# Optimization experiments

Hardware: AMD Instinct MI355X
Metric: run time of the kernel (lower is better)

Reference implementation:

```python
import jax, jax.numpy as jnp
import numpy as np

N, E, F, H = 50000, 800000, 128, 128

def silu(v):
    return v * jax.nn.sigmoid(v)

def setup_inputs() -> dict:
    key = jax.random.key(0)
    ks = jax.random.split(key, 16)
    def lin(k, fan_in, fan_out):
        s = 1.0 / np.sqrt(fan_in)
        kw, kb = jax.random.split(k)
        W = jax.random.uniform(kw, (fan_in, fan_out), jnp.float32, -s, s)
        b = jax.random.uniform(kb, (fan_out,), jnp.float32, -s, s)
        return W, b
    x = jax.random.normal(ks[0], (N, F), jnp.float32)
    pos = jax.random.normal(ks[1], (N, 3), jnp.float32)
    edge_index = jax.random.randint(ks[2], (2, E), 0, N, jnp.int64)
    We1, be1 = lin(ks[3], 2 * F + 1, H)
    We2, be2 = lin(ks[4], H, H)
    Wn1, bn1 = lin(ks[5], F + H, H)
    Wn2, bn2 = lin(ks[6], H, F)
    Wc, bc = lin(ks[7], H, 1)
    return {"x": x, "pos": pos, "We1": We1, "be1": be1, "We2": We2, "be2": be2,
            "Wn1": Wn1, "bn1": bn1, "Wn2": Wn2, "bn2": bn2, "Wc": Wc, "bc": bc,
            "edge_index": edge_index}

def reference(x, pos, We1, be1, We2, be2, Wn1, bn1, Wn2, bn2, Wc, bc, edge_index):
    row, col = edge_index[0], edge_index[1]
    rij = pos[row] - pos[col]                      # [E,3]
    dij = jnp.sum(rij ** 2, axis=-1, keepdims=True)  # [E,1]
    edge_input = jnp.concatenate([x[row], x[col], dij], axis=-1)  # [E,2F+1]
    m_ij = silu(silu(edge_input @ We1 + be1) @ We2 + be2)          # [E,H]
    agg = jax.ops.segment_sum(m_ij, row, num_segments=N)          # [N,H]
    x_new = silu(jnp.concatenate([x, agg], axis=-1) @ Wn1 + bn1) @ Wn2 + bn2  # [N,F]
    w_ij = silu(m_ij @ Wc + bc)                    # [E,1]
    trans = rij * w_ij                             # [E,3]
    delta = jax.ops.segment_sum(trans, row, num_segments=N)       # [N,3]
    pos_new = pos + 0.01 * delta
    return (x_new, pos_new)
```

## Files before the change

### kernel.cpp

```cpp
#include <hip/hip_runtime.h>
#include <hip/hip_bf16.h>
#include <stdint.h>
#include <string.h>

#define NN 50000
#define NE 800000
#define SCAN_B 200
#define SCAN_CH 250

typedef short bf8_t __attribute__((ext_vector_type(8)));
typedef float f32x4 __attribute__((ext_vector_type(4)));

__device__ __forceinline__ float silu_f(float v) {
    return v * __builtin_amdgcn_rcpf(1.0f + __expf(-v));
}

__device__ __forceinline__ unsigned int pack2bf(float a, float b) {
    __hip_bfloat162 h = __float22bfloat162_rn(make_float2(a, b));
    unsigned int u; memcpy(&u, &h, 4);
    return u;
}

__device__ __forceinline__ float bf_lo(unsigned int u) { return __uint_as_float(u << 16); }
__device__ __forceinline__ float bf_hi(unsigned int u) { return __uint_as_float(u & 0xffff0000u); }

union U4B { uint4 u; bf8_t b; };
__device__ __forceinline__ bf8_t as_bf8(uint4 u) { U4B x; x.u = u; return x.b; }

__global__ __launch_bounds__(64) void prep_w(const float* __restrict__ We1,
                                             const float* __restrict__ We2,
                                             const float* __restrict__ Wn1,
                                             const float* __restrict__ Wn2,
                                             unsigned short* __restrict__ wf1,
                                             unsigned short* __restrict__ wf2,
                                             unsigned short* __restrict__ wfn1,
                                             unsigned short* __restrict__ wfn2) {
    int b = blockIdx.x, lane = threadIdx.x;
    int q = lane >> 4, c = lane & 15;
    const float* W; unsigned short* dst; int f;
    if (b < 64)       { W = We1; f = b;       dst = wf1  + (size_t)f * 512; }
    else if (b < 96)  { W = We2; f = b - 64;  dst = wf2  + (size_t)f * 512; }
    else if (b < 160) { W = Wn1; f = b - 96;  dst = wfn1 + (size_t)f * 512; }
    else              { W = Wn2; f = b - 160; dst = wfn2 + (size_t)f * 512; }
    int s = f >> 3, mf = f & 7;
    int k0 = s * 32 + q * 8, col = mf * 16 + c;
    float v[8];
    #pragma unroll
    for (int i = 0; i < 8; ++i) v[i] = W[(size_t)(k0 + i) * 128 + col];
    uint4 o;
    o.x = pack2bf(v[0], v[1]); o.y = pack2bf(v[2], v[3]);
    o.z = pack2bf(v[4], v[5]); o.w = pack2bf(v[6], v[7]);
    *(uint4*)(dst + lane * 8) = o;
}

__device__ __forceinline__ void node_gemm_pass(
    const float* __restrict__ x, const unsigned* nb, const int* nloc, int n0,
    const char* __restrict__ wbase, const float* __restrict__ bias,
    unsigned short* __restrict__ dst, int P, int lane, int q, int oc_q)
{
    f32x4 acc[2][4];
    #pragma unroll
    for (int M = 0; M < 2; ++M) {
        float4 bi = bias ? *(const float4*)(bias + oc_q + M * 16) : make_float4(0.f, 0.f, 0.f, 0.f);
        #pragma unroll
        for (int t = 0; t < 4; ++t) { acc[M][t][0] = bi.x; acc[M][t][1] = bi.y; acc[M][t][2] = bi.z; acc[M][t][3] = bi.w; }
    }
    #pragma unroll
    for (int s = 0; s < 4; ++s) {
        bf8_t bfr[4];
        #pragma unroll
        for (int t = 0; t < 4; ++t) {
            const float* src = x + ((size_t)nb[t]) * 128 + s * 32 + q * 8;
            float4 v0 = *(const float4*)src;
            float4 v1 = *(const float4*)(src + 4);
            uint4 o;
            o.x = pack2bf(v0.x, v0.y); o.y = pack2bf(v0.z, v0.w);
            o.z = pack2bf(v1.x, v1.y); o.w = pack2bf(v1.z, v1.w);
            bfr[t] = as_bf8(o);
        }
        #pragma unroll
        for (int M = 0; M < 2; ++M) {
            unsigned woff = ((unsigned)(s * 8 + P * 2 + M) << 10) + ((unsigned)lane << 4);
            bf8_t af = as_bf8(*(const uint4*)(wbase + woff));
            #pragma unroll
            for (int t = 0; t < 4; ++t)
                acc[M][t] = __builtin_amdgcn_mfma_f32_16x16x32_bf16(af, bfr[t], acc[M][t], 0, 0, 0);
        }
    }
    #pragma unroll
    for (int M = 0; M < 2; ++M) {
        #pragma unroll
        for (int t = 0; t < 4; ++t) {
            int node = n0 + nloc[t];
            if (node < NN) {
                uint2 pz;
                pz.x = pack2bf(acc[M][t][0], acc[M][t][1]);
                pz.y = pack2bf(acc[M][t][2], acc[M][t][3]);
                *(uint2*)(dst + ((size_t)node << 7) + oc_q + M * 16) = pz;
            }
        }
    }
}

__global__ __launch_bounds__(256, 2) void prep_node(
    const float* __restrict__ x, const int* __restrict__ ei,
    const unsigned short* __restrict__ wf1, const unsigned short* __restrict__ wfn1,
    const float* __restrict__ be1, const float* __restrict__ bn1,
    unsigned short* __restrict__ zbf, unsigned short* __restrict__ ybf,
    unsigned short* __restrict__ znbf, int* __restrict__ cnt)
{
    const int tid = threadIdx.x;
    const int n0 = blockIdx.x * 64;

    {
        int e0 = (blockIdx.x * 256 + tid) * 4;
        if (e0 < NE) {
            int4 r4 = *(const int4*)(ei + e0);
            atomicAdd(&cnt[r4.x], 1); atomicAdd(&cnt[r4.y], 1);
            atomicAdd(&cnt[r4.z], 1); atomicAdd(&cnt[r4.w], 1);
        }
    }

    const int P = tid >> 6, lane = tid & 63;
    const int q = lane >> 4, e16 = lane & 15;
    const int oc_q = P * 32 + q * 4;

    int nloc[4]; unsigned nb[4];
    #pragma unroll
    for (int t = 0; t < 4; ++t) {
        int nl = t * 16 + e16; nloc[t] = nl;
        int node = n0 + nl; if (node >= NN) node = NN - 1;
        nb[t] = (unsigned)node;
    }

    node_gemm_pass(x, nb, nloc, n0, (const char*)wf1,           be1, zbf,  P, lane, q, oc_q);
    node_gemm_pass(x, nb, nloc, n0, (const char*)wf1 + (32u << 10), nullptr, ybf, P, lane, q, oc_q);
    node_gemm_pass(x, nb, nloc, n0, (const char*)wfn1,          bn1, znbf, P, lane, q, oc_q);
}

__global__ __launch_bounds__(256) void scan_bsum(const int* __restrict__ cnt,
                                                 int* __restrict__ bsum) {
    __shared__ int red[4];
    int b = blockIdx.x, tid = threadIdx.x;
    int n = b * SCAN_CH + tid;
    int v = (tid < SCAN_CH) ? cnt[n] : 0;
    #pragma unroll
    for (int o = 32; o; o >>= 1) v += __shfl_down(v, o);
    if ((tid & 63) == 0) red[tid >> 6] = v;
    __syncthreads();
    if (tid == 0) bsum[b] = red[0] + red[1] + red[2] + red[3];
}

__global__ __launch_bounds__(256) void scan_write(const int* __restrict__ cnt,
                                                  const int* __restrict__ bsum,
                                                  int* __restrict__ off,
                                                  int* __restrict__ cur) {
    __shared__ int part[256];
    __shared__ int basered[4];
    int b = blockIdx.x, tid = threadIdx.x;
    int bv = (tid < b) ? bsum[tid] : 0;
    #pragma unroll
    for (int o = 32; o; o >>= 1) bv += __shfl_down(bv, o);
    if ((tid & 63) == 0) basered[tid >> 6] = bv;
    __syncthreads();
    int base = basered[0] + basered[1] + basered[2] + basered[3];
    int n = b * SCAN_CH + tid;
    int c = (tid < SCAN_CH) ? cnt[n] : 0;
    part[tid] = c;
    __syncthreads();
    #pragma unroll
    for (int d = 1; d < 256; d <<= 1) {
        int v = (tid >= d) ? part[tid - d] : 0;
        __syncthreads();
        part[tid] += v;
        __syncthreads();
    }
    if (tid < SCAN_CH) {
        int excl = base + part[tid] - c;
        off[n] = excl; cur[n] = excl;
    }
    if (b == SCAN_B - 1 && tid == SCAN_CH) off[NN] = NE;
}

__global__ __launch_bounds__(256) void egnn_scatter(const int* __restrict__ ei,
                                                    int* __restrict__ cur,
                                                    int2* __restrict__ rc_slot) {
    int e = (blockIdx.x * 256 + threadIdx.x) * 4;
    if (e < NE) {
        int4 r4 = *(const int4*)(ei + e);
        int4 c4 = *(const int4*)(ei + NE + e);
        int p0 = atomicAdd(&cur[r4.x], 1); rc_slot[p0] = make_int2(r4.x, c4.x);
        int p1 = atomicAdd(&cur[r4.y], 1); rc_slot[p1] = make_int2(r4.y, c4.y);
        int p2 = atomicAdd(&cur[r4.z], 1); rc_slot[p2] = make_int2(r4.z, c4.z);
        int p3 = atomicAdd(&cur[r4.w], 1); rc_slot[p3] = make_int2(r4.w, c4.w);
    }
}

__global__ __launch_bounds__(256, 5) void egnn_edge_mfma(
    const unsigned short* __restrict__ zbf, const unsigned short* __restrict__ ybf,
    const float* __restrict__ pos,
    const unsigned short* __restrict__ wf2,
    const float* __restrict__ We1,
    const float* __restrict__ be2, const float* __restrict__ Wc,
    const float* __restrict__ bc,
    const int2* __restrict__ rc_slot,
    float* __restrict__ agg, float* __restrict__ delta)
{
    __shared__ __align__(16) unsigned short HsBuf[9216];
    unsigned short* Hs = HsBuf;
    unsigned short* mT = HsBuf;
    __shared__ int   rows_s[64];
    __shared__ float rij_s[64][3];
    __shared__ float dij_s[64];
    __shared__ float wdot[64];
    __shared__ int   seg_node[64], seg_start[65];
    __shared__ unsigned long long smask;
    __shared__ int firstPartial, lastPartial;

    const int tid = threadIdx.x;
    const int bid = blockIdx.x;
    const int xcd = bid & 7, ii = bid >> 3;
    const int blk = (xcd < 4 ? xcd * 1563 : 4 * 1563 + (xcd - 4) * 1562) + ii;
    const int e0 = blk * 64;
    const char* zb = (const char*)zbf;
    const char* yb = (const char*)ybf;
    const char* w2 = (const char*)wf2;

    if (tid < 64) {
        int2 rc = rc_slot[e0 + tid];
        int r = rc.x;
        rows_s[tid] = r;
        float d = 0.f;
        #pragma unroll
        for (int k = 0; k < 3; ++k) {
            float rv = pos[r * 3 + k] - pos[rc.y * 3 + k];
            rij_s[tid][k] = rv; d += rv * rv;
        }
        dij_s[tid] = d;
        wdot[tid] = 0.f;
        seg_start[tid] = 64;
        if (tid == 0) seg_start[64] = 64;
        int prev = __shfl_up(r, 1);
        bool flag = (tid == 0) || (r != prev);
        unsigned long long b = __ballot(flag);
        int seg = __popcll(b & ((2ull << tid) - 1)) - 1;
        if (flag) { seg_node[seg] = r; seg_start[seg] = tid; }
        int r63 = __shfl(r, 63);
        if (tid == 0) {
            smask = b;
            firstPartial = (e0 > 0) && (rc_slot[e0 - 1].x == r);
            lastPartial  = (e0 + 64 < NE) && (rc_slot[e0 + 64].x == r63);
        }
    }

    const int P = tid >> 6, lane = tid & 63;
    const int q = lane >> 4, e16 = lane & 15;
    const int oc_q = P * 32 + q * 4;

    int eloc[4]; unsigned rb[4], cb[4];
    #pragma unroll
    for (int t = 0; t < 4; ++t) {
        int el = t * 16 + e16; eloc[t] = el;
        int2 rc = rc_slot[e0 + el];
        rb[t] = (unsigned)rc.x << 8;
        cb[t] = (unsigned)rc.y << 8;
    }

    uint2 uzr[2][4], uyr[2][4];
    #pragma unroll
    for (int M = 0; M < 2; ++M) {
        const unsigned cbyte = (unsigned)((oc_q + M * 16) << 1);
        #pragma unroll
        for (int t = 0; t < 4; ++t) {
            uzr[M][t] = *(const uint2*)(zb + rb[t] + cbyte);
            uyr[M][t] = *(const uint2*)(yb + cb[t] + cbyte);
        }
    }
    __syncthreads();

    #pragma unroll
    for (int M = 0; M < 2; ++M) {
        float4 w256 = *(const float4*)(We1 + (size_t)256 * 128 + oc_q + M * 16);
        #pragma unroll
        for (int t = 0; t < 4; ++t) {
            uint2 uz = uzr[M][t], uy = uyr[M][t];
            float d = dij_s[eloc[t]];
            float v0 = silu_f(bf_lo(uz.x) + bf_lo(uy.x) + d * w256.x);
            float v1 = silu_f(bf_hi(uz.x) + bf_hi(uy.x) + d * w256.y);
            float v2 = silu_f(bf_lo(uz.y) + bf_lo(uy.y) + d * w256.z);
            float v3 = silu_f(bf_hi(uz.y) + bf_hi(uy.y) + d * w256.w);
            uint2 pk; pk.x = pack2bf(v0, v1); pk.y = pack2bf(v2, v3);
            *(uint2*)(Hs + eloc[t] * 136 + oc_q + M * 16) = pk;
        }
    }
    __syncthreads();

    f32x4 acc2[2][4];
    #pragma unroll
    for (int M = 0; M < 2; ++M) {
        float4 bi = *(const float4*)(be2 + oc_q + M * 16);
        #pragma unroll
        for (int t = 0; t < 4; ++t) { acc2[M][t][0] = bi.x; acc2[M][t][1] = bi.y; acc2[M][t][2] = bi.z; acc2[M][t][3] = bi.w; }
    }

    #pragma unroll
    for (int s = 0; s < 4; ++s) {
        bf8_t bfr[4];
        #pragma unroll
        for (int t = 0; t < 4; ++t)
            bfr[t] = as_bf8(*(const uint4*)(Hs + eloc[t] * 136 + s * 32 + q * 8));
        __builtin_amdgcn_s_setprio(1);
        #pragma unroll
        for (int M = 0; M < 2; ++M) {
            unsigned woff = ((unsigned)(s * 8 + P * 2 + M) << 10) + ((unsigned)lane << 4);
            bf8_t af = as_bf8(*(const uint4*)(w2 + woff));
            #pragma unroll
            for (int t = 0; t < 4; ++t)
                acc2[M][t] = __builtin_amdgcn_mfma_f32_16x16x32_bf16(af, bfr[t], acc2[M][t], 0, 0, 0);
        }
        __builtin_amdgcn_s_setprio(0);
    }
    __syncthreads();

    {
        float4 wcA = *(const float4*)(Wc + oc_q);
        float4 wcB = *(const float4*)(Wc + oc_q + 16);
        float part[4];
        #pragma unroll
        for (int t = 0; t < 4; ++t) part[t] = 0.f;

        #pragma unroll
        for (int M = 0; M < 2; ++M) {
            float4 wc = (M == 0) ? wcA : wcB;
            int cbase = oc_q + M * 16;
            #pragma unroll
            for (int t = 0; t < 4; ++t) {
                float v0 = silu_f(acc2[M][t][0]);
                float v1 = silu_f(acc2[M][t][1]);
                float v2 = silu_f(acc2[M][t][2]);
                float v3 = silu_f(acc2[M][t][3]);
                part[t] += v0 * wc.x + v1 * wc.y + v2 * wc.z + v3 * wc.w;
                unsigned ua = pack2bf(v0, v1), ub = pack2bf(v2, v3);
                int slot = eloc[t];
                mT[(cbase + 0) * 72 + slot] = (unsigned short)ua;
                mT[(cbase + 1) * 72 + slot] = (unsigned short)(ua >> 16);
                mT[(cbase + 2) * 72 + slot] = (unsigned short)ub;
                mT[(cbase + 3) * 72 + slot] = (unsigned short)(ub >> 16);
            }
        }
        #pragma unroll
        for (int t = 0; t < 4; ++t) {
            float p = part[t];
            p += __shfl_xor(p, 16);
            p += __shfl_xor(p, 32);
            if (q == 0) atomicAdd(&wdot[eloc[t]], p);
        }
    }
    __syncthreads();

    {
        const int wv = tid >> 6, l = tid & 63;
        const int cA = l & 15, kq = l >> 4;
        const int nseg = __popcll(smask);

        if (nseg <= 16) {
            const int st = seg_start[cA];
            const int en = seg_start[cA + 1];
            f32x4 accd[2];
            #pragma unroll
            for (int c2 = 0; c2 < 2; ++c2) { accd[c2][0] = 0.f; accd[c2][1] = 0.f; accd[c2][2] = 0.f; accd[c2][3] = 0.f; }
            #pragma unroll
            for (int kt = 0; kt < 2; ++kt) {
                bf8_t aS;
                #pragma unroll
                for (int i = 0; i < 8; ++i) {
                    int k = kt * 32 + kq * 8 + i;
                    aS[i] = (k >= st && k < en) ? (short)0x3F80 : (short)0;
                }
                #pragma unroll
                for (int c2 = 0; c2 < 2; ++c2) {
                    int ct = wv * 2 + c2;
                    bf8_t bM = as_bf8(*(const uint4*)(mT + (ct * 16 + cA) * 72 + kt * 32 + kq * 8));
                    accd[c2] = __builtin_amdgcn_mfma_f32_16x16x32_bf16(aS, bM, accd[c2], 0, 0, 0);
                }
            }
            #pragma unroll
            for (int c2 = 0; c2 < 2; ++c2) {
                int ct = wv * 2 + c2;
                #pragma unroll
                for (int r = 0; r < 4; ++r) {
                    int sg = kq * 4 + r;
                    if (sg < nseg) {
                        float v = accd[c2][r];
                        int node = seg_node[sg];
                        bool partial = (sg == 0 && firstPartial) || (sg == nseg - 1 && lastPartial);
                        float* dst = agg + (size_t)node * 128 + ct * 16 + cA;
                        if (partial) atomicAdd(dst, v); else *dst = v;
                    }
                }
            }
        } else if (wv * 16 < nseg) {
            const int seg = wv * 16 + cA;
            const int st = seg_start[seg];
            const int en = seg_start[seg + 1];
            f32x4 accd[8];
            #pragma unroll
            for (int ct = 0; ct < 8; ++ct) { accd[ct][0] = 0.f; accd[ct][1] = 0.f; accd[ct][2] = 0.f; accd[ct][3] = 0.f; }
            #pragma unroll
            for (int kt = 0; kt < 2; ++kt) {
                bf8_t aS;
                #pragma unroll
                for (int i = 0; i < 8; ++i) {
                    int k = kt * 32 + kq * 8 + i;
                    aS[i] = (k >= st && k < en) ? (short)0x3F80 : (short)0;
                }
                #pragma unroll
                for (int ct = 0; ct < 8; ++ct) {
                    bf8_t bM = as_bf8(*(const uint4*)(mT + (ct * 16 + cA) * 72 + kt * 32 + kq * 8));
                    accd[ct] = __builtin_amdgcn_mfma_f32_16x16x32_bf16(aS, bM, accd[ct], 0, 0, 0);
                }
            }
            #pragma unroll
            for (int ct = 0; ct < 8; ++ct) {
                #pragma unroll
                for (int r = 0; r < 4; ++r) {
                    int sg = wv * 16 + kq * 4 + r;
                    if (sg < nseg) {
                        float v = accd[ct][r];
                        int node = seg_node[sg];
                        bool partial = (sg == 0 && firstPartial) || (sg == nseg - 1 && lastPartial);
                        float* dst = agg + (size_t)node * 128 + ct * 16 + cA;
                        if (partial) atomicAdd(dst, v); else *dst = v;
                    }
                }
            }
        }

        if (tid < nseg) {
            float bcv = bc[0];
            int start = seg_start[tid];
            int end = (tid + 1 < nseg) ? seg_start[tid + 1] : 64;
            float d0 = 0.f, d1 = 0.f, d2 = 0.f;
            for (int s2 = start; s2 < end; ++s2) {
                float wgt = silu_f(wdot[s2] + bcv);
                d0 += rij_s[s2][0] * wgt;
                d1 += rij_s[s2][1] * wgt;
                d2 += rij_s[s2][2] * wgt;
            }
            int node = seg_node[tid];
            bool partial = (tid == 0 && firstPartial) || (tid == nseg - 1 && lastPartial);
            float* dd = delta + (size_t)node * 3;
            if (partial) { atomicAdd(dd, d0); atomicAdd(dd + 1, d1); atomicAdd(dd + 2, d2); }
            else         { dd[0] = d0; dd[1] = d1; dd[2] = d2; }
        }
    }
}

__global__ __launch_bounds__(256, 4) void egnn_node_mfma(
    const unsigned short* __restrict__ znbf, const float* __restrict__ agg,
    const float* __restrict__ delta, const float* __restrict__ pos,
    const unsigned short* __restrict__ wfn1, const unsigned short* __restrict__ wfn2,
    const float* __restrict__ bn2,
    float* __restrict__ out)
{
    __shared__ unsigned short Hs[64 * 136];

    const int tid = threadIdx.x;
    const int n0 = blockIdx.x * 64;
    const char* zn = (const char*)znbf;
    const char* ab = (const char*)agg;
    const char* w1 = (const char*)wfn1;
    const char* w2 = (const char*)wfn2;

    if (tid < 192) {
        int n = n0 + tid / 3, d = tid - 3 * (tid / 3);
        if (n < NN)
            out[(size_t)NN * 128 + (size_t)n * 3 + d] =
                pos[(size_t)n * 3 + d] + 0.01f * delta[(size_t)n * 3 + d];
    }

    const int P = tid >> 6, lane = tid & 63;
    const int q = lane >> 4, e16 = lane & 15;
    const int oc_q = P * 32 + q * 4;

    int nloc[4]; unsigned nb[4];
    #pragma unroll
    for (int t = 0; t < 4; ++t) {
        int nl = t * 16 + e16; nloc[t] = nl;
        int node = n0 + nl; if (node >= NN) node = NN - 1;
        nb[t] = (unsigned)node;
    }

    f32x4 acc[2][4];
    #pragma unroll
    for (int M = 0; M < 2; ++M) {
        const unsigned cbyte = (unsigned)((oc_q + M * 16) << 1);
        #pragma unroll
        for (int t = 0; t < 4; ++t) {
            uint2 uz = *(const uint2*)(zn + (nb[t] << 8) + cbyte);
            acc[M][t][0] = bf_lo(uz.x); acc[M][t][1] = bf_hi(uz.x);
            acc[M][t][2] = bf_lo(uz.y); acc[M][t][3] = bf_hi(uz.y);
        }
    }

    #pragma unroll
    for (int s = 0; s < 4; ++s) {
        bf8_t bfr[4];
        #pragma unroll
        for (int t = 0; t < 4; ++t) {
            unsigned aoff = (nb[t] << 9) + (unsigned)((s * 32 + q * 8) * 4);
            float4 a0 = *(const float4*)(ab + aoff);
            float4 a1 = *(const float4*)(ab + aoff + 16);
            uint4 o;
            o.x = pack2bf(a0.x, a0.y); o.y = pack2bf(a0.z, a0.w);
            o.z = pack2bf(a1.x, a1.y); o.w = pack2bf(a1.z, a1.w);
            bfr[t] = as_bf8(o);
        }
        #pragma unroll
        for (int M = 0; M < 2; ++M) {
            unsigned woff = ((unsigned)((s + 4) * 8 + P * 2 + M) << 10) + ((unsigned)lane << 4);
            bf8_t af = as_bf8(*(const uint4*)(w1 + woff));
            #pragma unroll
            for (int t = 0; t < 4; ++t)
                acc[M][t] = __builtin_amdgcn_mfma_f32_16x16x32_bf16(af, bfr[t], acc[M][t], 0, 0, 0);
        }
    }

    #pragma unroll
    for (int M = 0; M < 2; ++M) {
        #pragma unroll
        for (int t = 0; t < 4; ++t) {
            float v0 = silu_f(acc[M][t][0]);
            float v1 = silu_f(acc[M][t][1]);
            float v2 = silu_f(acc[M][t][2]);
            float v3 = silu_f(acc[M][t][3]);
            uint2 pk; pk.x = pack2bf(v0, v1); pk.y = pack2bf(v2, v3);
            *(uint2*)(Hs + nloc[t] * 136 + oc_q + M * 16) = pk;
        }
    }
    __syncthreads();

    f32x4 acc2[2][4];
    #pragma unroll
    for (int M = 0; M < 2; ++M) {
        float4 bi = *(const float4*)(bn2 + oc_q + M * 16);
        #pragma unroll
        for (int t = 0; t < 4; ++t) { acc2[M][t][0] = bi.x; acc2[M][t][1] = bi.y; acc2[M][t][2] = bi.z; acc2[M][t][3] = bi.w; }
    }

    #pragma unroll
    for (int s = 0; s < 4; ++s) {
        bf8_t bfr[4];
        #pragma unroll
        for (int t = 0; t < 4; ++t)
            bfr[t] = as_bf8(*(const uint4*)(Hs + nloc[t] * 136 + s * 32 + q * 8));
        #pragma unroll
        for (int M = 0; M < 2; ++M) {
            unsigned woff = ((unsigned)(s * 8 + P * 2 + M) << 10) + ((unsigned)lane << 4);
            bf8_t af = as_bf8(*(const uint4*)(w2 + woff));
            #pragma unroll
            for (int t = 0; t < 4; ++t)
                acc2[M][t] = __builtin_amdgcn_mfma_f32_16x16x32_bf16(af, bfr[t], acc2[M][t], 0, 0, 0);
        }
    }

    #pragma unroll
    for (int M = 0; M < 2; ++M) {
        #pragma unroll
        for (int t = 0; t < 4; ++t) {
            int node = n0 + nloc[t];
            if (node < NN) {
                float4 v; v.x = acc2[M][t][0]; v.y = acc2[M][t][1]; v.z = acc2[M][t][2]; v.w = acc2[M][t][3];
                *(float4*)(out + (size_t)node * 128 + oc_q + M * 16) = v;
            }
        }
    }
}

extern "C" void kernel_launch(void* const* d_in, const int* in_sizes, int n_in,
                              void* d_out, int out_size, void* d_ws, size_t ws_size,
                              hipStream_t stream)
{
    const float* x   = (const float*)d_in[0];
    const float* pos = (const float*)d_in[1];
    const float* We1 = (const float*)d_in[2];
    const float* be1 = (const float*)d_in[3];
    const float* We2 = (const float*)d_in[4];
    const float* be2 = (const float*)d_in[5];
    const float* Wn1 = (const float*)d_in[6];
    const float* bn1 = (const float*)d_in[7];
    const float* Wn2 = (const float*)d_in[8];
    const float* bn2 = (const float*)d_in[9];
    const float* Wc  = (const float*)d_in[10];
    const float* bc  = (const float*)d_in[11];
    const int*   ei  = (const int*)d_in[12];
    float* out = (float*)d_out;

    char* p = (char*)d_ws;
    float* agg   = (float*)p;                  p += (size_t)NN * 128 * 4;
    float* delta = (float*)p;                  p += (size_t)NN * 3 * 4;
    int* cnt     = (int*)p;                    p += (size_t)NN * 4;
    unsigned short* znbf = (unsigned short*)p; p += (size_t)NN * 128 * 2;
    unsigned short* zbf = (unsigned short*)p;  p += (size_t)NN * 128 * 2;
    unsigned short* ybf = (unsigned short*)p;  p += (size_t)NN * 128 * 2;
    unsigned short* wf1  = (unsigned short*)p; p += 65536;
    unsigned short* wf2  = (unsigned short*)p; p += 32768;
    unsigned short* wfn1 = (unsigned short*)p; p += 65536;
    unsigned short* wfn2 = (unsigned short*)p; p += 32768;
    int* off   = (int*)p;                      p += (size_t)(NN + 1) * 4 + 12;
    int* cur   = (int*)p;                      p += (size_t)NN * 4;
    int* bsum  = (int*)p;                      p += (size_t)SCAN_B * 4;
    int2* rc_slot = (int2*)p;

    hipMemsetAsync(agg, 0, ((size_t)NN * 128 + (size_t)NN * 3 + NN) * 4, stream);

    prep_w<<<192, 64, 0, stream>>>(We1, We2, Wn1, Wn2, wf1, wf2, wfn1, wfn2);
    prep_node<<<(NN + 63) / 64, 256, 0, stream>>>(x, ei, wf1, wfn1, be1, bn1,
                                                  zbf, ybf, znbf, cnt);
    scan_bsum<<<SCAN_B, 256, 0, stream>>>(cnt, bsum);
    scan_write<<<SCAN_B, 256, 0, stream>>>(cnt, bsum, off, cur);
    egnn_scatter<<<(NE / 4 + 255) / 256, 256, 0, stream>>>(ei, cur, rc_slot);
    egnn_edge_mfma<<<NE / 64, 256, 0, stream>>>(zbf, ybf, pos, wf2, We1, be2,
                                                Wc, bc, rc_slot, agg, delta);
    egnn_node_mfma<<<(NN + 63) / 64, 256, 0, stream>>>(znbf, agg, delta, pos,
                                                       wfn1, wfn2, bn2, out);
}
```

Before: 294.5 us.

## Fuse three node GEMM passes and precompute edge distances in scatter

The three node-side GEMM passes in prep_node are merged into one loop, so each x tile is loaded and converted to bf16 once and feeds three sets of MFMA accumulators. The scatter kernel now computes each edge's squared distance and stores it in a widened int4 slot. The edge kernel issues its z/y gathers before the shared-memory setup and drops one __syncthreads. This trades more registers (the edge kernel's occupancy hint drops from 5 to 4) and a larger rc_slot buffer for fewer global reads and less synchronization.

```diff
diff --git a/kernel.cpp b/kernel.cpp
--- a/kernel.cpp
+++ b/kernel.cpp
@@ -53,55 +53,6 @@
     *(uint4*)(dst + lane * 8) = o;
 }
 
-__device__ __forceinline__ void node_gemm_pass(
-    const float* __restrict__ x, const unsigned* nb, const int* nloc, int n0,
-    const char* __restrict__ wbase, const float* __restrict__ bias,
-    unsigned short* __restrict__ dst, int P, int lane, int q, int oc_q)
-{
-    f32x4 acc[2][4];
-    #pragma unroll
-    for (int M = 0; M < 2; ++M) {
-        float4 bi = bias ? *(const float4*)(bias + oc_q + M * 16) : make_float4(0.f, 0.f, 0.f, 0.f);
-        #pragma unroll
-        for (int t = 0; t < 4; ++t) { acc[M][t][0] = bi.x; acc[M][t][1] = bi.y; acc[M][t][2] = bi.z; acc[M][t][3] = bi.w; }
-    }
-    #pragma unroll
-    for (int s = 0; s < 4; ++s) {
-        bf8_t bfr[4];
-        #pragma unroll
-        for (int t = 0; t < 4; ++t) {
-            const float* src = x + ((size_t)nb[t]) * 128 + s * 32 + q * 8;
-            float4 v0 = *(const float4*)src;
-            float4 v1 = *(const float4*)(src + 4);
-            uint4 o;
-            o.x = pack2bf(v0.x, v0.y); o.y = pack2bf(v0.z, v0.w);
-            o.z = pack2bf(v1.x, v1.y); o.w = pack2bf(v1.z, v1.w);
-            bfr[t] = as_bf8(o);
-        }
-        #pragma unroll
-        for (int M = 0; M < 2; ++M) {
-            unsigned woff = ((unsigned)(s * 8 + P * 2 + M) << 10) + ((unsigned)lane << 4);
-            bf8_t af = as_bf8(*(const uint4*)(wbase + woff));
-            #pragma unroll
-            for (int t = 0; t < 4; ++t)
-                acc[M][t] = __builtin_amdgcn_mfma_f32_16x16x32_bf16(af, bfr[t], acc[M][t], 0, 0, 0);
-        }
-    }
-    #pragma unroll
-    for (int M = 0; M < 2; ++M) {
-        #pragma unroll
-        for (int t = 0; t < 4; ++t) {
-            int node = n0 + nloc[t];
-            if (node < NN) {
-                uint2 pz;
-                pz.x = pack2bf(acc[M][t][0], acc[M][t][1]);
-                pz.y = pack2bf(acc[M][t][2], acc[M][t][3]);
-                *(uint2*)(dst + ((size_t)node << 7) + oc_q + M * 16) = pz;
-            }
-        }
-    }
-}
-
 __global__ __launch_bounds__(256, 2) void prep_node(
     const float* __restrict__ x, const int* __restrict__ ei,
     const unsigned short* __restrict__ wf1, const unsigned short* __restrict__ wfn1,
@@ -111,6 +62,8 @@
 {
     const int tid = threadIdx.x;
     const int n0 = blockIdx.x * 64;
+    const char* w1 = (const char*)wf1;
+    const char* wn = (const char*)wfn1;
 
     {
         int e0 = (blockIdx.x * 256 + tid) * 4;
@@ -133,9 +86,64 @@
         nb[t] = (unsigned)node;
     }
 
-    node_gemm_pass(x, nb, nloc, n0, (const char*)wf1,           be1, zbf,  P, lane, q, oc_q);
-    node_gemm_pass(x, nb, nloc, n0, (const char*)wf1 + (32u << 10), nullptr, ybf, P, lane, q, oc_q);
-    node_gemm_pass(x, nb, nloc, n0, (const char*)wfn1,          bn1, znbf, P, lane, q, oc_q);
+    f32x4 az[2][4], ay[2][4], an[2][4];
+    #pragma unroll
+    for (int M = 0; M < 2; ++M) {
+        float4 b1 = *(const float4*)(be1 + oc_q + M * 16);
+        float4 b2 = *(const float4*)(bn1 + oc_q + M * 16);
+        #pragma unroll
+        for (int t = 0; t < 4; ++t) {
+            az[M][t][0] = b1.x; az[M][t][1] = b1.y; az[M][t][2] = b1.z; az[M][t][3] = b1.w;
+            ay[M][t][0] = 0.f;  ay[M][t][1] = 0.f;  ay[M][t][2] = 0.f;  ay[M][t][3] = 0.f;
+            an[M][t][0] = b2.x; an[M][t][1] = b2.y; an[M][t][2] = b2.z; an[M][t][3] = b2.w;
+        }
+    }
+
+    #pragma unroll
+    for (int s = 0; s < 4; ++s) {
+        bf8_t bfr[4];
+        #pragma unroll
+        for (int t = 0; t < 4; ++t) {
+            const float* src = x + ((size_t)nb[t]) * 128 + s * 32 + q * 8;
+            float4 v0 = *(const float4*)src;
+            float4 v1 = *(const float4*)(src + 4);
+            uint4 o;
+            o.x = pack2bf(v0.x, v0.y); o.y = pack2bf(v0.z, v0.w);
+            o.z = pack2bf(v1.x, v1.y); o.w = pack2bf(v1.z, v1.w);
+            bfr[t] = as_bf8(o);
+        }
+        #pragma unroll
+        for (int M = 0; M < 2; ++M) {
+            unsigned wz = ((unsigned)(s * 8 + P * 2 + M) << 10) + ((unsigned)lane << 4);
+            unsigned wy = ((unsigned)((s + 4) * 8 + P * 2 + M) << 10) + ((unsigned)lane << 4);
+            bf8_t afz = as_bf8(*(const uint4*)(w1 + wz));
+            bf8_t afy = as_bf8(*(const uint4*)(w1 + wy));
+            bf8_t afn = as_bf8(*(const uint4*)(wn + wz));
+            #pragma unroll
+            for (int t = 0; t < 4; ++t) {
+                az[M][t] = __builtin_amdgcn_mfma_f32_16x16x32_bf16(afz, bfr[t], az[M][t], 0, 0, 0);
+                ay[M][t] = __builtin_amdgcn_mfma_f32_16x16x32_bf16(afy, bfr[t], ay[M][t], 0, 0, 0);
+                an[M][t] = __builtin_amdgcn_mfma_f32_16x16x32_bf16(afn, bfr[t], an[M][t], 0, 0, 0);
+            }
+        }
+    }
+
+    #pragma unroll
+    for (int M = 0; M < 2; ++M) {
+        #pragma unroll
+        for (int t = 0; t < 4; ++t) {
+            int node = n0 + nloc[t];
+            if (node < NN) {
+                uint2 pz, py, pn;
+                pz.x = pack2bf(az[M][t][0], az[M][t][1]); pz.y = pack2bf(az[M][t][2], az[M][t][3]);
+                py.x = pack2bf(ay[M][t][0], ay[M][t][1]); py.y = pack2bf(ay[M][t][2], ay[M][t][3]);
+                pn.x = pack2bf(an[M][t][0], an[M][t][1]); pn.y = pack2bf(an[M][t][2], an[M][t][3]);
+                *(uint2*)(zbf  + ((size_t)node << 7) + oc_q + M * 16) = pz;
+                *(uint2*)(ybf  + ((size_t)node << 7) + oc_q + M * 16) = py;
+                *(uint2*)(znbf + ((size_t)node << 7) + oc_q + M * 16) = pn;
+            }
+        }
+    }
 }
 
 __global__ __launch_bounds__(256) void scan_bsum(const int* __restrict__ cnt,
@@ -183,35 +191,41 @@
 }
 
 __global__ __launch_bounds__(256) void egnn_scatter(const int* __restrict__ ei,
+                                                    const float* __restrict__ pos,
                                                     int* __restrict__ cur,
-                                                    int2* __restrict__ rc_slot) {
+                                                    int4* __restrict__ rc_slot) {
     int e = (blockIdx.x * 256 + threadIdx.x) * 4;
     if (e < NE) {
         int4 r4 = *(const int4*)(ei + e);
         int4 c4 = *(const int4*)(ei + NE + e);
-        int p0 = atomicAdd(&cur[r4.x], 1); rc_slot[p0] = make_int2(r4.x, c4.x);
-        int p1 = atomicAdd(&cur[r4.y], 1); rc_slot[p1] = make_int2(r4.y, c4.y);
-        int p2 = atomicAdd(&cur[r4.z], 1); rc_slot[p2] = make_int2(r4.z, c4.z);
-        int p3 = atomicAdd(&cur[r4.w], 1); rc_slot[p3] = make_int2(r4.w, c4.w);
-    }
-}
-
-__global__ __launch_bounds__(256, 5) void egnn_edge_mfma(
+        #pragma unroll
+        for (int j = 0; j < 4; ++j) {
+            int r = (j == 0) ? r4.x : (j == 1) ? r4.y : (j == 2) ? r4.z : r4.w;
+            int c = (j == 0) ? c4.x : (j == 1) ? c4.y : (j == 2) ? c4.z : c4.w;
+            float dx = pos[r * 3 + 0] - pos[c * 3 + 0];
+            float dy = pos[r * 3 + 1] - pos[c * 3 + 1];
+            float dz = pos[r * 3 + 2] - pos[c * 3 + 2];
+            float d = dx * dx + dy * dy + dz * dz;
+            int p = atomicAdd(&cur[r], 1);
+            rc_slot[p] = make_int4(r, c, __float_as_int(d), 0);
+        }
+    }
+}
+
+__global__ __launch_bounds__(256, 4) void egnn_edge_mfma(
     const unsigned short* __restrict__ zbf, const unsigned short* __restrict__ ybf,
     const float* __restrict__ pos,
     const unsigned short* __restrict__ wf2,
     const float* __restrict__ We1,
     const float* __restrict__ be2, const float* __restrict__ Wc,
     const float* __restrict__ bc,
-    const int2* __restrict__ rc_slot,
+    const int4* __restrict__ rc_slot,
     float* __restrict__ agg, float* __restrict__ delta)
 {
     __shared__ __align__(16) unsigned short HsBuf[9216];
     unsigned short* Hs = HsBuf;
     unsigned short* mT = HsBuf;
-    __shared__ int   rows_s[64];
     __shared__ float rij_s[64][3];
-    __shared__ float dij_s[64];
     __shared__ float wdot[64];
     __shared__ int   seg_node[64], seg_start[65];
     __shared__ unsigned long long smask;
@@ -226,17 +240,37 @@
     const char* yb = (const char*)ybf;
     const char* w2 = (const char*)wf2;
 
+    const int P = tid >> 6, lane = tid & 63;
+    const int q = lane >> 4, e16 = lane & 15;
+    const int oc_q = P * 32 + q * 4;
+
+    int eloc[4]; unsigned rb[4], cb[4]; float dijt[4];
+    #pragma unroll
+    for (int t = 0; t < 4; ++t) {
+        int el = t * 16 + e16; eloc[t] = el;
+        int4 sl = rc_slot[e0 + el];
+        rb[t] = (unsigned)sl.x << 8;
+        cb[t] = (unsigned)sl.y << 8;
+        dijt[t] = __int_as_float(sl.z);
+    }
+
+    uint2 uzr[2][4], uyr[2][4];
+    #pragma unroll
+    for (int M = 0; M < 2; ++M) {
+        const unsigned cbyte = (unsigned)((oc_q + M * 16) << 1);
+        #pragma unroll
+        for (int t = 0; t < 4; ++t) {
+            uzr[M][t] = *(const uint2*)(zb + rb[t] + cbyte);
+            uyr[M][t] = *(const uint2*)(yb + cb[t] + cbyte);
+        }
+    }
+
     if (tid < 64) {
-        int2 rc = rc_slot[e0 + tid];
-        int r = rc.x;
-        rows_s[tid] = r;
-        float d = 0.f;
-        #pragma unroll
-        for (int k = 0; k < 3; ++k) {
-            float rv = pos[r * 3 + k] - pos[rc.y * 3 + k];
-            rij_s[tid][k] = rv; d += rv * rv;
-        }
-        dij_s[tid] = d;
+        int4 sl = rc_slot[e0 + tid];
+        int r = sl.x;
+        #pragma unroll
+        for (int k = 0; k < 3; ++k)
+            rij_s[tid][k] = pos[r * 3 + k] - pos[sl.y * 3 + k];
         wdot[tid] = 0.f;
         seg_start[tid] = 64;
         if (tid == 0) seg_start[64] = 64;
@@ -253,38 +287,13 @@
         }
     }
 
-    const int P = tid >> 6, lane = tid & 63;
-    const int q = lane >> 4, e16 = lane & 15;
-    const int oc_q = P * 32 + q * 4;
-
-    int eloc[4]; unsigned rb[4], cb[4];
-    #pragma unroll
-    for (int t = 0; t < 4; ++t) {
-        int el = t * 16 + e16; eloc[t] = el;
-        int2 rc = rc_slot[e0 + el];
-        rb[t] = (unsigned)rc.x << 8;
-        cb[t] = (unsigned)rc.y << 8;
-    }
-
-    uint2 uzr[2][4], uyr[2][4];
-    #pragma unroll
-    for (int M = 0; M < 2; ++M) {
-        const unsigned cbyte = (unsigned)((oc_q + M * 16) << 1);
-        #pragma unroll
-        for (int t = 0; t < 4; ++t) {
-            uzr[M][t] = *(const uint2*)(zb + rb[t] + cbyte);
-            uyr[M][t] = *(const uint2*)(yb + cb[t] + cbyte);
-        }
-    }
-    __syncthreads();
-
     #pragma unroll
     for (int M = 0; M < 2; ++M) {
         float4 w256 = *(const float4*)(We1 + (size_t)256 * 128 + oc_q + M * 16);
         #pragma unroll
         for (int t = 0; t < 4; ++t) {
             uint2 uz = uzr[M][t], uy = uyr[M][t];
-            float d = dij_s[eloc[t]];
+            float d = dijt[t];
             float v0 = silu_f(bf_lo(uz.x) + bf_lo(uy.x) + d * w256.x);
             float v1 = silu_f(bf_hi(uz.x) + bf_hi(uy.x) + d * w256.y);
             float v2 = silu_f(bf_lo(uz.y) + bf_lo(uy.y) + d * w256.z);
@@ -609,8 +618,8 @@
     unsigned short* wfn2 = (unsigned short*)p; p += 32768;
     int* off   = (int*)p;                      p += (size_t)(NN + 1) * 4 + 12;
     int* cur   = (int*)p;                      p += (size_t)NN * 4;
-    int* bsum  = (int*)p;                      p += (size_t)SCAN_B * 4;
-    int2* rc_slot = (int2*)p;
+    int* bsum  = (int*)p;                      p += (size_t)SCAN_B * 4 + 48;
+    int4* rc_slot = (int4*)p;
 
     hipMemsetAsync(agg, 0, ((size_t)NN * 128 + (size_t)NN * 3 + NN) * 4, stream);
 
@@ -619,7 +628,7 @@
                                                   zbf, ybf, znbf, cnt);
     scan_bsum<<<SCAN_B, 256, 0, stream>>>(cnt, bsum);
     scan_write<<<SCAN_B, 256, 0, stream>>>(cnt, bsum, off, cur);
-    egnn_scatter<<<(NE / 4 + 255) / 256, 256, 0, stream>>>(ei, cur, rc_slot);
+    egnn_scatter<<<(NE / 4 + 255) / 256, 256, 0, stream>>>(ei, pos, cur, rc_slot);
     egnn_edge_mfma<<<NE / 64, 256, 0, stream>>>(zbf, ybf, pos, wf2, We1, be2,
                                                 Wc, bc, rc_slot, agg, delta);
     egnn_node_mfma<<<(NN + 63) / 64, 256, 0, stream>>>(znbf, agg, delta, pos,
```

After: 289.6 us. Within noise of the previous version (-1.6%).
